# Optimization experiments

Hardware: AMD Instinct MI355X
Metric: run time of the kernel (lower is better)

## Reference

```python
import jax, jax.numpy as jnp
import numpy as np

N_FFT = 2048
HOP = 512


def _hann(n):
    # scipy.signal.get_window('hann', n, fftbins=True)
    return (0.5 - 0.5 * np.cos(2.0 * np.pi * np.arange(n) / n)).astype(np.float32)


def setup_inputs() -> dict:
    key = jax.random.key(0)
    k1, k2 = jax.random.split(key)
    B, T, F = 8, 1000, N_FFT // 2 + 1
    real_stft = jax.random.normal(k1, (B, 1, T, F), dtype=jnp.float32)
    imag_stft = jax.random.normal(k2, (B, 1, T, F), dtype=jnp.float32)

    # Windowed IDFT matrices, exactly as ISTFT.__init__ builds conv weights.
    n = N_FFT
    x, y = np.meshgrid(np.arange(n), np.arange(n))
    ang = 2.0 * np.pi * ((x * y) % n) / n  # angle of omega**(x*y), omega = exp(2*pi*i/n)
    win = _hann(n)  # win_length == n_fft -> pad_center is a no-op
    W_real = (np.cos(ang) / n * win[:, None]).astype(np.float32)
    W_imag = (np.sin(ang) / n * win[:, None]).astype(np.float32)

    return {
        "real_stft": real_stft,
        "imag_stft": imag_stft,
        "W_real": jnp.asarray(W_real),
        "W_imag": jnp.asarray(W_imag),
        "window": jnp.asarray(win),
        "length": 511488,  # HOP * (n_frames - 1) with n_frames = 1000
    }


def reference(real_stft, imag_stft, W_real, W_imag, window, length):
    n_fft, hop = N_FFT, HOP
    B = real_stft.shape[0]

    fr = jnp.swapaxes(real_stft[:, 0], 1, 2)  # (B, n_fft//2+1, T)
    fi = jnp.swapaxes(imag_stft[:, 0], 1, 2)
    # Hermitian symmetry -> full (B, n_fft, T) spectrum
    full_r = jnp.concatenate([fr, jnp.flip(fr[:, 1:-1, :], axis=1)], axis=1)
    full_i = jnp.concatenate([fi, -jnp.flip(fi[:, 1:-1, :], axis=1)], axis=1)

    # center=True and length given (static Python int)
    padded_length = length + n_fft
    n_frames = min(fr.shape[2], -(-padded_length // hop))

    # windowed real IFFT per frame: s[b, o, t]
    s = (jnp.einsum('oi,bit->bot', W_real, full_r[:, :, :n_frames])
         - jnp.einsum('oi,bit->bot', W_imag, full_i[:, :, :n_frames]))

    L = n_fft + hop * (n_frames - 1)
    # fused overlap-add via scatter-add
    idx = (jnp.arange(n_frames)[:, None] * hop + jnp.arange(n_fft)[None, :]).reshape(-1)
    frames = jnp.swapaxes(s, 1, 2).reshape(B, -1)  # (B, n_frames*n_fft)
    y = jnp.zeros((B, L), s.dtype).at[:, idx].add(frames)

    # window sum-square normalization (librosa.filters.window_sumsquare)
    wss = jnp.zeros((L,), window.dtype).at[idx].add(jnp.tile(window ** 2, n_frames))
    tiny = jnp.finfo(window.dtype).tiny
    nz = wss > tiny
    y = jnp.where(nz[None, :], y / jnp.where(nz, wss, 1.0)[None, :], y)

    start = n_fft // 2
    return y[:, start:start + length]
```

## Files before the change

### kernel.cpp

```cpp
#include <hip/hip_runtime.h>


#define N_FFT    2048
#define HOP      512
#define T_FRAMES 1000
#define F_BINS   1025
#define OUT_LEN  511488
#define FPB      4
#define BPB      250
#define OAF      3584

#define P(a) ((a) + ((a) >> 4))

__device__ __forceinline__ void cmul(float ar, float ai, float br, float bi,
                                     float& cr, float& ci) {
    cr = ar * br - ai * bi;
    ci = ar * bi + ai * br;
}

__global__ __launch_bounds__(256, 4) void istft_oa_kernel(const float* __restrict__ re,
                                                          const float* __restrict__ im,
                                                          const float* __restrict__ win,
                                                          float* __restrict__ scratch,
                                                          float* __restrict__ out) {
    __shared__ __align__(16) float2 buf[1088];
    __shared__ __align__(16) float2 oa2[OAF / 2];

    const int j   = blockIdx.x;
    const int b   = blockIdx.y;
    const int tid = threadIdx.x;
    const int t0  = j * FPB;

    {
        float4* z4 = (float4*)oa2;
        #pragma unroll
        for (int e = 0; e < 4; ++e) {
            int idx = tid + 256 * e;
            if (idx < 896) z4[idx] = make_float4(0.f, 0.f, 0.f, 0.f);
        }
    }

    float pcs[4], psn[4];
    #pragma unroll
    for (int q = 0; q < 4; ++q) {
        float ang = 3.14159265358979f * (float)(tid + 256 * q) / 1024.f;
        __sincosf(ang, &psn[q], &pcs[q]);
    }
    float tc1[4], ts1[4], tc2[4], ts2[4], tc3[4], ts3[4];
    #pragma unroll
    for (int s = 1; s < 4; ++s) {
        const int hm = 1 << (2 * s);
        const int jj = tid & (hm - 1);
        float ang = 1.57079632679f * (float)jj / (float)hm;
        __sincosf(ang, &ts1[s - 1], &tc1[s - 1]);
        cmul(tc1[s-1], ts1[s-1], tc1[s-1], ts1[s-1], tc2[s-1], ts2[s-1]);
        cmul(tc2[s-1], ts2[s-1], tc1[s-1], ts1[s-1], tc3[s-1], ts3[s-1]);
    }
    {
        float ang = 1.57079632679f * (float)tid / 256.f;
        __sincosf(ang, &ts1[3], &tc1[3]);
        cmul(tc1[3], ts1[3], tc1[3], ts1[3], tc2[3], ts2[3]);
        cmul(tc2[3], ts2[3], tc1[3], ts1[3], tc3[3], ts3[3]);
    }

    const float Sc = 0.5f / 1024.f;
    const float2* w2v = (const float2*)win;

    for (int d = 0; d < FPB; ++d) {
        const int f = b * T_FRAMES + t0 + d;
        const float* fr = re + (size_t)f * F_BINS;
        const float* fi = im + (size_t)f * F_BINS;

        #pragma unroll
        for (int q = 0; q < 4; ++q) {
            int k = 256 * q + tid;
            float ar = fr[k];
            float ai = (k == 0) ? 0.f : fi[k];
            int mk = 1024 - k;
            float br = fr[mk];
            float bi = (mk == 1024) ? 0.f : fi[mk];
            float dr = ar - br, di = ai + bi;
            float cs = pcs[q], sn = psn[q];
            float Zr = (ar + br - (cs * di + sn * dr)) * Sc;
            float Zi = (ai - bi + (cs * dr - sn * di)) * Sc;
            unsigned r10 = __brev((unsigned)k) >> 22;
            int rk = (int)(((r10 & 0x155u) << 1) | ((r10 >> 1) & 0x155u));
            buf[P(rk)] = make_float2(Zr, Zi);
        }
        __syncthreads();

        {
            int base = tid << 2;
            int i0 = P(base), i1 = P(base + 1), i2 = P(base + 2), i3 = P(base + 3);
            float2 a = buf[i0], bb = buf[i1], c = buf[i2], dd = buf[i3];
            float t0r = a.x + c.x,  t0i = a.y + c.y;
            float t1r = a.x - c.x,  t1i = a.y - c.y;
            float t2r = bb.x + dd.x, t2i = bb.y + dd.y;
            float t3r = bb.x - dd.x, t3i = bb.y - dd.y;
            buf[i0] = make_float2(t0r + t2r, t0i + t2i);
            buf[i1] = make_float2(t1r - t3i, t1i + t3r);
            buf[i2] = make_float2(t0r - t2r, t0i - t2i);
            buf[i3] = make_float2(t1r + t3i, t1i - t3r);
        }

        #pragma unroll
        for (int s = 1; s < 4; ++s) {
            __builtin_amdgcn_wave_barrier();
            const int hm = 1 << (2 * s);
            const int jj   = tid & (hm - 1);
            const int base = ((tid - jj) << 2) + jj;
            const float c1 = tc1[s-1], s1v = ts1[s-1];
            const float c2 = tc2[s-1], s2v = ts2[s-1];
            const float c3 = tc3[s-1], s3v = ts3[s-1];

            int i0 = P(base), i1 = P(base + hm), i2 = P(base + 2 * hm), i3 = P(base + 3 * hm);
            float2 a = buf[i0], bb = buf[i1], c = buf[i2], dd = buf[i3];
            float br_, bi_, cr_, ci_, dr_, di_;
            cmul(bb.x, bb.y, c1, s1v, br_, bi_);
            cmul(c.x,  c.y,  c2, s2v, cr_, ci_);
            cmul(dd.x, dd.y, c3, s3v, dr_, di_);

            float t0r = a.x + cr_, t0i = a.y + ci_;
            float t1r = a.x - cr_, t1i = a.y - ci_;
            float t2r = br_ + dr_, t2i = bi_ + di_;
            float t3r = br_ - dr_, t3i = bi_ - di_;
            buf[i0] = make_float2(t0r + t2r, t0i + t2i);
            buf[i1] = make_float2(t1r - t3i, t1i + t3r);
            buf[i2] = make_float2(t0r - t2r, t0i - t2i);
            buf[i3] = make_float2(t1r + t3i, t1i - t3r);
        }
        __syncthreads();

        {
            const float c1 = tc1[3], s1v = ts1[3];
            const float c2 = tc2[3], s2v = ts2[3];
            const float c3 = tc3[3], s3v = ts3[3];

            int i0 = P(tid), i1 = P(tid + 256), i2 = P(tid + 512), i3 = P(tid + 768);
            float2 a = buf[i0], bb = buf[i1], c = buf[i2], dd = buf[i3];
            float br_, bi_, cr_, ci_, dr_, di_;
            cmul(bb.x, bb.y, c1, s1v, br_, bi_);
            cmul(c.x,  c.y,  c2, s2v, cr_, ci_);
            cmul(dd.x, dd.y, c3, s3v, dr_, di_);

            float t0r = a.x + cr_, t0i = a.y + ci_;
            float t1r = a.x - cr_, t1i = a.y - ci_;
            float t2r = br_ + dr_, t2i = bi_ + di_;
            float t3r = br_ - dr_, t3i = bi_ - di_;

            float2 z0 = make_float2(t0r + t2r, t0i + t2i);
            float2 z1 = make_float2(t1r - t3i, t1i + t3r);
            float2 z2 = make_float2(t0r - t2r, t0i - t2i);
            float2 z3 = make_float2(t1r + t3i, t1i - t3r);

            float2 w0 = w2v[tid],       w1 = w2v[tid + 256];
            float2 w2 = w2v[tid + 512], w3 = w2v[tid + 768];

            const int base2 = 256 * d;
            float2 v;
            v = oa2[base2 + tid];
            v.x += z0.x * w0.x;  v.y += z0.y * w0.y;
            oa2[base2 + tid] = v;
            v = oa2[base2 + tid + 256];
            v.x += z1.x * w1.x;  v.y += z1.y * w1.y;
            oa2[base2 + tid + 256] = v;
            v = oa2[base2 + tid + 512];
            v.x += z2.x * w2.x;  v.y += z2.y * w2.y;
            oa2[base2 + tid + 512] = v;
            v = oa2[base2 + tid + 768];
            v.x += z3.x * w3.x;  v.y += z3.y * w3.y;
            oa2[base2 + tid + 768] = v;
        }
        __syncthreads();
    }

    const float inv = 2.f / 3.f;
    const float4* oa4 = (const float4*)oa2;
    if (tid < 128) {
        float4 v = oa4[384 + tid];
        float4* o4 = (float4*)(out + (size_t)b * OUT_LEN + (size_t)2048 * j + 512);
        o4[tid] = make_float4(v.x * inv, v.y * inv, v.z * inv, v.w * inv);
    }
    float4* sc4 = (float4*)(scratch + (((size_t)b * BPB + j) * 2) * 1536);
    #pragma unroll
    for (int e = 0; e < 3; ++e) {
        int idx = tid + 256 * e;
        float4 v = (idx < 384) ? oa4[idx] : oa4[idx + 128];
        sc4[idx] = v;
    }
}

__global__ __launch_bounds__(256) void seam_kernel(const float* __restrict__ scratch,
                                                   const float* __restrict__ win,
                                                   float* __restrict__ out) {
    const int g = blockIdx.x;
    const int b = blockIdx.y;

    #pragma unroll
    for (int e = 0; e < 6; ++e) {
        int i = threadIdx.x + 256 * e;
        int n = 2048 * g + i;
        int m = n - 1024;
        if (m < 0 || m >= OUT_LEN) continue;
        float s = 0.f;
        if (g > 0)
            s += scratch[(((size_t)b * BPB + (g - 1)) * 2 + 1) * 1536 + i];
        if (g < BPB)
            s += scratch[(((size_t)b * BPB + g) * 2) * 1536 + i];
        float r;
        if (n >= 1536 && n < 512000) {
            r = s * (2.f / 3.f);
        } else {
            int thi = n >> 9; if (thi > T_FRAMES - 1) thi = T_FRAMES - 1;
            int tlo = (n - (N_FFT - HOP)) >> 9; if (tlo < 0) tlo = 0;
            float wss = 0.f;
            for (int t = tlo; t <= thi; ++t) {
                float w = win[n - (t << 9)];
                wss += w * w;
            }
            r = (wss > 1.17549435e-38f) ? s / wss : s;
        }
        out[(size_t)b * OUT_LEN + m] = r;
    }
}

extern "C" void kernel_launch(void* const* d_in, const int* in_sizes, int n_in,
                              void* d_out, int out_size, void* d_ws, size_t ws_size,
                              hipStream_t stream) {
    const float* re  = (const float*)d_in[0];
    const float* im  = (const float*)d_in[1];
    const float* win = (const float*)d_in[4];
    float* out = (float*)d_out;

    float* scratch = (float*)d_ws;

    istft_oa_kernel<<<dim3(BPB, 8), 256, 0, stream>>>(re, im, win, scratch, out);
    seam_kernel<<<dim3(BPB + 1, 8), 256, 0, stream>>>(scratch, win, out);
}
```

Measured before the change: 145.1 us.

## Fuse first radix-4 FFT stage into load phase and hoist window loads

```diff
diff --git a/kernel.cpp b/kernel.cpp
--- a/kernel.cpp
+++ b/kernel.cpp
@@ -40,17 +40,22 @@
         }
     }
 
+    const unsigned r8 = __brev((unsigned)tid) >> 24;
+    const int m = (int)(((r8 & 0x55u) << 1) | ((r8 >> 1) & 0x55u));
+
     float pcs[4], psn[4];
     #pragma unroll
     for (int q = 0; q < 4; ++q) {
         float ang = 3.14159265358979f * (float)(tid + 256 * q) / 1024.f;
         __sincosf(ang, &psn[q], &pcs[q]);
     }
+    const int j1 = (tid >> 4) & 3;
+    const int g1 = (tid & 15) | (((tid >> 6) & 3) << 4);
     float tc1[4], ts1[4], tc2[4], ts2[4], tc3[4], ts3[4];
     #pragma unroll
     for (int s = 1; s < 4; ++s) {
         const int hm = 1 << (2 * s);
-        const int jj = tid & (hm - 1);
+        const int jj = (s == 1) ? j1 : (tid & (hm - 1));
         float ang = 1.57079632679f * (float)jj / (float)hm;
         __sincosf(ang, &ts1[s - 1], &tc1[s - 1]);
         cmul(tc1[s-1], ts1[s-1], tc1[s-1], ts1[s-1], tc2[s-1], ts2[s-1]);
@@ -62,15 +67,18 @@
         cmul(tc1[3], ts1[3], tc1[3], ts1[3], tc2[3], ts2[3]);
         cmul(tc2[3], ts2[3], tc1[3], ts1[3], tc3[3], ts3[3]);
     }
+    const float2* w2v = (const float2*)win;
+    const float2 hw0 = w2v[tid],       hw1 = w2v[tid + 256];
+    const float2 hw2 = w2v[tid + 512], hw3 = w2v[tid + 768];
 
     const float Sc = 0.5f / 1024.f;
-    const float2* w2v = (const float2*)win;
 
     for (int d = 0; d < FPB; ++d) {
         const int f = b * T_FRAMES + t0 + d;
         const float* fr = re + (size_t)f * F_BINS;
         const float* fi = im + (size_t)f * F_BINS;
 
+        float zr[4], zi[4];
         #pragma unroll
         for (int q = 0; q < 4; ++q) {
             int k = 256 * q + tid;
@@ -81,34 +89,32 @@
             float bi = (mk == 1024) ? 0.f : fi[mk];
             float dr = ar - br, di = ai + bi;
             float cs = pcs[q], sn = psn[q];
-            float Zr = (ar + br - (cs * di + sn * dr)) * Sc;
-            float Zi = (ai - bi + (cs * dr - sn * di)) * Sc;
-            unsigned r10 = __brev((unsigned)k) >> 22;
-            int rk = (int)(((r10 & 0x155u) << 1) | ((r10 >> 1) & 0x155u));
-            buf[P(rk)] = make_float2(Zr, Zi);
+            zr[q] = (ar + br - (cs * di + sn * dr)) * Sc;
+            zi[q] = (ai - bi + (cs * dr - sn * di)) * Sc;
+        }
+        {
+            float t0r = zr[0] + zr[2], t0i = zi[0] + zi[2];
+            float t1r = zr[0] - zr[2], t1i = zi[0] - zi[2];
+            float t2r = zr[1] + zr[3], t2i = zi[1] + zi[3];
+            float t3r = zr[1] - zr[3], t3i = zi[1] - zi[3];
+            buf[P(4 * m + 0)] = make_float2(t0r + t2r, t0i + t2i);
+            buf[P(4 * m + 1)] = make_float2(t1r - t3i, t1i + t3r);
+            buf[P(4 * m + 2)] = make_float2(t0r - t2r, t0i - t2i);
+            buf[P(4 * m + 3)] = make_float2(t1r + t3i, t1i - t3r);
         }
         __syncthreads();
-
-        {
-            int base = tid << 2;
-            int i0 = P(base), i1 = P(base + 1), i2 = P(base + 2), i3 = P(base + 3);
-            float2 a = buf[i0], bb = buf[i1], c = buf[i2], dd = buf[i3];
-            float t0r = a.x + c.x,  t0i = a.y + c.y;
-            float t1r = a.x - c.x,  t1i = a.y - c.y;
-            float t2r = bb.x + dd.x, t2i = bb.y + dd.y;
-            float t3r = bb.x - dd.x, t3i = bb.y - dd.y;
-            buf[i0] = make_float2(t0r + t2r, t0i + t2i);
-            buf[i1] = make_float2(t1r - t3i, t1i + t3r);
-            buf[i2] = make_float2(t0r - t2r, t0i - t2i);
-            buf[i3] = make_float2(t1r + t3i, t1i - t3r);
-        }
 
         #pragma unroll
         for (int s = 1; s < 4; ++s) {
             __builtin_amdgcn_wave_barrier();
             const int hm = 1 << (2 * s);
-            const int jj   = tid & (hm - 1);
-            const int base = ((tid - jj) << 2) + jj;
+            int base;
+            if (s == 1) {
+                base = 16 * g1 + j1;
+            } else {
+                const int jj = tid & (hm - 1);
+                base = ((tid - jj) << 2) + jj;
+            }
             const float c1 = tc1[s-1], s1v = ts1[s-1];
             const float c2 = tc2[s-1], s2v = ts2[s-1];
             const float c3 = tc3[s-1], s3v = ts3[s-1];
@@ -153,22 +159,19 @@
             float2 z2 = make_float2(t0r - t2r, t0i - t2i);
             float2 z3 = make_float2(t1r + t3i, t1i - t3r);
 
-            float2 w0 = w2v[tid],       w1 = w2v[tid + 256];
-            float2 w2 = w2v[tid + 512], w3 = w2v[tid + 768];
-
             const int base2 = 256 * d;
             float2 v;
             v = oa2[base2 + tid];
-            v.x += z0.x * w0.x;  v.y += z0.y * w0.y;
+            v.x += z0.x * hw0.x;  v.y += z0.y * hw0.y;
             oa2[base2 + tid] = v;
             v = oa2[base2 + tid + 256];
-            v.x += z1.x * w1.x;  v.y += z1.y * w1.y;
+            v.x += z1.x * hw1.x;  v.y += z1.y * hw1.y;
             oa2[base2 + tid + 256] = v;
             v = oa2[base2 + tid + 512];
-            v.x += z2.x * w2.x;  v.y += z2.y * w2.y;
+            v.x += z2.x * hw2.x;  v.y += z2.y * hw2.y;
             oa2[base2 + tid + 512] = v;
             v = oa2[base2 + tid + 768];
-            v.x += z3.x * w3.x;  v.y += z3.y * w3.y;
+            v.x += z3.x * hw3.x;  v.y += z3.y * hw3.y;
             oa2[base2 + tid + 768] = v;
         }
         __syncthreads();
```

Measured after the change: 140.4 us. 1.03x faster.
